# Kernel tuning notes

Hardware: AMD Instinct MI355X
Metric: run time of the kernel (lower is better)

The kernel has to match this reference:

```python
import jax, jax.numpy as jnp
import numpy as np

H = 1024      # hidden_size
NH = 16       # num_heads
HD = H // NH  # head_dim


def setup_inputs() -> dict:
    key = jax.random.key(0)
    ks = jax.random.split(key, 12)
    inp = {
        "query": jax.random.normal(ks[0], (4, 1024, H), dtype=jnp.float32),
        "key": jax.random.normal(ks[1], (4, 2048, H), dtype=jnp.float32),
        "value": jax.random.normal(ks[2], (4, 2048, H), dtype=jnp.float32),
        "key_padding_mask": jax.random.randint(ks[3], (4, 2048), 0, 2, dtype=jnp.int32),
        # learned parameters (torch Linear: y = x @ W.T + b); we store W already transposed
        "Wq": jax.random.normal(ks[4], (H, H), dtype=jnp.float32) * (1.0 / np.sqrt(H)),
        "bq": jnp.zeros((H,), dtype=jnp.float32),
        "Wk": jax.random.normal(ks[5], (H, H), dtype=jnp.float32) * (1.0 / np.sqrt(H)),
        "bk": jnp.zeros((H,), dtype=jnp.float32),
        "Wv": jax.random.normal(ks[6], (H, H), dtype=jnp.float32) * (1.0 / np.sqrt(H)),
        "bv": jnp.zeros((H,), dtype=jnp.float32),
        "Wo": jax.random.normal(ks[7], (H, H), dtype=jnp.float32) * (1.0 / np.sqrt(H)),
        "bo": jnp.zeros((H,), dtype=jnp.float32),
    }
    return inp


def reference(query, key, value, key_padding_mask, Wq, bq, Wk, bk, Wv, bv, Wo, bo):
    B, Sq, _ = query.shape
    Sk = key.shape[1]
    scaling = HD ** -0.5
    # projections -> [B, NH, S, HD]
    q = (query @ Wq + bq).reshape(B, Sq, NH, HD).transpose(0, 2, 1, 3)
    k = (key @ Wk + bk).reshape(B, Sk, NH, HD).transpose(0, 2, 1, 3)
    v = (value @ Wv + bv).reshape(B, Sk, NH, HD).transpose(0, 2, 1, 3)
    # scores [B, NH, Sq, Sk]
    scores = jnp.einsum("bhqd,bhkd->bhqk", q, k) * scaling
    # mask: positions where key_padding_mask == 0 are ignored
    scores = jnp.where((key_padding_mask == 0)[:, None, None, :], -jnp.inf, scores)
    attn = jax.nn.softmax(scores, axis=-1)
    # dropout is identity in eval mode
    out = jnp.einsum("bhqk,bhkd->bhqd", attn, v)
    out = out.transpose(0, 2, 1, 3).reshape(B, Sq, H)
    return out @ Wo + bo
```

## Files before the change

kernel.cpp:

```cpp
#include <hip/hip_runtime.h>
#include <hip/hip_fp16.h>
#include <math.h>

#define B_ 4
#define SQ 1024
#define SK 2048
#define HH 1024
#define NHEAD 16
#define HDIM 64

typedef _Float16 f16;
typedef __attribute__((ext_vector_type(8))) _Float16 f16x8;
typedef __attribute__((ext_vector_type(4))) _Float16 f16x4;
typedef __attribute__((ext_vector_type(4))) float f32x4;
typedef unsigned int u32;

#define GLOAD_LDS16(gp, lp) __builtin_amdgcn_global_load_lds( \
    (const __attribute__((address_space(1))) u32*)(gp),        \
    (__attribute__((address_space(3))) u32*)(lp), 16, 0, 0)
#define GLOAD_LDS4(gp, lp) __builtin_amdgcn_global_load_lds(  \
    (const __attribute__((address_space(1))) u32*)(gp),        \
    (__attribute__((address_space(3))) u32*)(lp), 4, 0, 0)

__global__ __launch_bounds__(256) void prep_k(
    const float* __restrict__ q, const float* __restrict__ k,
    const float* __restrict__ v,
    const float* __restrict__ W0, const float* __restrict__ W1,
    const float* __restrict__ W2, const float* __restrict__ W3,
    const int* __restrict__ mask,
    f16* __restrict__ qo, f16* __restrict__ ko, f16* __restrict__ vo,
    f16* __restrict__ WT, float* __restrict__ pbias)
{
    __shared__ f16 t[64 * 80];
    const int bid = blockIdx.x, tid = threadIdx.x;
    if (bid < 10240) {
        int i = bid * 256 + tid;
        const float* src; f16* dst; int j;
        if (i < 524288)       { src = q; dst = qo; j = i; }
        else if (i < 1572864) { src = k; dst = ko; j = i - 524288; }
        else                  { src = v; dst = vo; j = i - 1572864; }
        float4 a = ((const float4*)src)[(size_t)j * 2];
        float4 b = ((const float4*)src)[(size_t)j * 2 + 1];
        f16x8 o;
        o[0] = (f16)a.x; o[1] = (f16)a.y; o[2] = (f16)a.z; o[3] = (f16)a.w;
        o[4] = (f16)b.x; o[5] = (f16)b.y; o[6] = (f16)b.z; o[7] = (f16)b.w;
        *(f16x8*)(dst + (size_t)j * 8) = o;
    } else if (bid < 11264) {
        int id = bid - 10240;
        int z = id >> 8, idx = id & 255;
        const float* W = z == 0 ? W0 : z == 1 ? W1 : z == 2 ? W2 : W3;
        f16* out = WT + (size_t)z * HH * HH;
        const int r0 = (idx >> 4) * 64, c0 = (idx & 15) * 64;
#pragma unroll
        for (int p = 0; p < 4; p++) {
            int s = p * 256 + tid;
            int row = s >> 4, u = s & 15;
            float4 a = *(const float4*)(W + (size_t)(r0 + row) * HH + c0 + u * 4);
            f16x4 vv;
            vv[0] = (f16)a.x; vv[1] = (f16)a.y; vv[2] = (f16)a.z; vv[3] = (f16)a.w;
            *(f16x4*)(t + row * 80 + u * 4) = vv;
        }
        __syncthreads();
#pragma unroll
        for (int p = 0; p < 2; p++) {
            int s = p * 256 + tid;
            int n = s >> 3, u = s & 7;
            f16x8 vv;
#pragma unroll
            for (int j = 0; j < 8; j++) vv[j] = t[(u * 8 + j) * 80 + n];
            *(f16x8*)(out + (size_t)(c0 + n) * HH + r0 + u * 8) = vv;
        }
    } else {
        int j = (bid - 11264) * 256 + tid;
        pbias[j] = mask[j] ? 0.f : -1e30f;
    }
}

template <int TM, int OUTMODE>
__device__ __forceinline__ void gemm_body(
    const f16* __restrict__ A, const f16* __restrict__ BT,
    const float* __restrict__ bias, void* __restrict__ Cout,
    int M, int bid, int nwg, f16* sA, f16* sB)
{
    const int tid = threadIdx.x, lane = tid & 63, w = tid >> 6;
    const int swz = (bid & 7) * (nwg >> 3) + (bid >> 3);
    const int m0 = (swz >> 3) * TM;
    const int n0 = (swz & 7) * 128;
    const int wr = w >> 1, wc = w & 1;
    const int ql = lane & 15, g = lane >> 4;
    const int N = 1024, K = 1024;
    const int MF = TM / 32;
    const int ABUF = TM * 32;
    f32x4 acc[TM / 32][4] = {};

    auto stage = [&](int buf, int k0) {
#pragma unroll
        for (int p = 0; p < TM / 64; p++) {
            int s = p * 256 + tid;
            int row = s >> 2, us = ((s & 3) ^ ((row >> 1) & 3)) * 8;
            GLOAD_LDS16(A + (size_t)(m0 + row) * K + k0 + us,
                        sA + buf * ABUF + (p * 256 + w * 64) * 8);
        }
#pragma unroll
        for (int p = 0; p < 2; p++) {
            int s = p * 256 + tid;
            int row = s >> 2, us = ((s & 3) ^ ((row >> 1) & 3)) * 8;
            GLOAD_LDS16(BT + (size_t)(n0 + row) * K + k0 + us,
                        sB + buf * 4096 + (p * 256 + w * 64) * 8);
        }
    };

    stage(0, 0);
    int cur = 0;
    for (int k0 = 0; k0 < K; k0 += 32) {
        __syncthreads();
        if (k0 + 32 < K) stage(cur ^ 1, k0 + 32);
        f16x8 af[MF], bf[4];
#pragma unroll
        for (int m = 0; m < MF; m++) {
            int row = wr * (TM / 2) + m * 16 + ql;
            af[m] = *(const f16x8*)(sA + cur * ABUF + row * 32 + ((g ^ ((row >> 1) & 3)) * 8));
        }
#pragma unroll
        for (int n = 0; n < 4; n++) {
            int row = wc * 64 + n * 16 + ql;
            bf[n] = *(const f16x8*)(sB + cur * 4096 + row * 32 + ((g ^ ((row >> 1) & 3)) * 8));
        }
#pragma unroll
        for (int m = 0; m < MF; m++)
#pragma unroll
            for (int n = 0; n < 4; n++)
                acc[m][n] = __builtin_amdgcn_mfma_f32_16x16x32_f16(af[m], bf[n], acc[m][n], 0, 0, 0);
        cur ^= 1;
    }

    float bv[4];
#pragma unroll
    for (int n = 0; n < 4; n++) bv[n] = bias[n0 + wc * 64 + n * 16 + ql];
#pragma unroll
    for (int m = 0; m < MF; m++) {
        int row0 = m0 + wr * (TM / 2) + m * 16 + g * 4;
#pragma unroll
        for (int n = 0; n < 4; n++) {
            int col = n0 + wc * 64 + n * 16 + ql;
            if (OUTMODE == 2) {
                int bb = row0 >> 11, kk = row0 & 2047;
                int hh = col >> 6, dd = col & 63;
                f16x4 vv;
#pragma unroll
                for (int e = 0; e < 4; e++) vv[e] = (f16)(acc[m][n][e] + bv[n]);
                *(f16x4*)((f16*)Cout + ((size_t)(bb * NHEAD + hh) * HDIM + dd) * SK + kk) = vv;
            } else if (OUTMODE == 1) {
#pragma unroll
                for (int e = 0; e < 4; e++)
                    ((f16*)Cout)[(size_t)(row0 + e) * N + col] = (f16)(acc[m][n][e] + bv[n]);
            } else {
#pragma unroll
                for (int e = 0; e < 4; e++)
                    ((float*)Cout)[(size_t)(row0 + e) * N + col] = acc[m][n][e] + bv[n];
            }
        }
    }
}

__global__ __launch_bounds__(256) void qkv_gemm_k(
    const f16* __restrict__ qc, const f16* __restrict__ kc,
    const f16* __restrict__ vc, const f16* __restrict__ wT,
    const float* __restrict__ bq, const float* __restrict__ bk,
    const float* __restrict__ bv,
    f16* __restrict__ qp, f16* __restrict__ kp, f16* __restrict__ vt)
{
    __shared__ f16 sA[2 * 4096];
    __shared__ f16 sB[2 * 4096];
    const int bid = blockIdx.x;
    const size_t M1 = 1024 * 1024;
    if (bid < 512)
        gemm_body<64, 1>(qc, wT, bq, qp, 4096, bid, 512, sA, sB);
    else if (bid < 1024)
        gemm_body<128, 1>(kc, wT + M1, bk, kp, 8192, bid - 512, 512, sA, sB);
    else
        gemm_body<128, 2>(vc, wT + 2 * M1, bv, vt, 8192, bid - 1024, 512, sA, sB);
}

__global__ __launch_bounds__(256) void o_gemm_k(
    const f16* __restrict__ ctx, const f16* __restrict__ wT,
    const float* __restrict__ bo, float* __restrict__ out)
{
    __shared__ f16 sA[2 * 4096];
    __shared__ f16 sB[2 * 4096];
    gemm_body<64, 0>(ctx, wT, bo, out, 4096, blockIdx.x, 512, sA, sB);
}

#define SC2 0.18033688f
#define THR2 11.5f

__global__ __launch_bounds__(512, 6) void attn_mfma_k(
    const f16* __restrict__ qp,
    const f16* __restrict__ kp,
    const f16* __restrict__ vt,
    const float* __restrict__ pbias,
    f16* __restrict__ ctx)
{
    const int flat = ((int)blockIdx.x & 7) * 64 + ((int)blockIdx.x >> 3);
    const int qt = flat & 7, h = (flat >> 3) & 15, b = flat >> 7;
    const int q0 = qt * 128;
    const int tid = threadIdx.x, lane = tid & 63, w = tid >> 6;
    const int ql = lane & 15, g = lane >> 4;

    __shared__ f16 ks[2 * 4096];
    __shared__ f16 vs[2 * 4096];
    __shared__ f16 plds[8][16 * 80];
    __shared__ float sbias[2][64];

    const f16* kbase = kp + (size_t)b * SK * HH + h * HDIM;
    const f16* vbase = vt + ((size_t)(b * NHEAD + h)) * HDIM * SK;
    const float* bbase = pbias + b * SK;

    f16x8 qf[2];
    {
        const f16* qb = qp + ((size_t)(b * SQ + q0 + w * 16 + ql)) * HH + h * HDIM + g * 8;
        qf[0] = *(const f16x8*)qb;
        qf[1] = *(const f16x8*)(qb + 32);
    }

    auto stageKV = [&](int buf, int kt) {
        int r = tid >> 3, ulg = ((tid & 7) ^ (r & 7)) * 8;
        GLOAD_LDS16(kbase + (size_t)(kt + r) * HH + ulg, ks + buf * 4096 + w * 512);
        GLOAD_LDS16(vbase + (size_t)r * SK + kt + ulg,   vs + buf * 4096 + w * 512);
        if (w == 0) GLOAD_LDS4(bbase + kt + lane, &sbias[buf][0]);
    };

    f32x4 oacc[4] = {};
    float mrun = -1e30f, lrun = 0.f;

    stageKV(0, 0);
    int cur = 0;
    for (int kt = 0; kt < SK; kt += 64) {
        __syncthreads();
        if (kt + 64 < SK) stageKV(cur ^ 1, kt + 64);
        const f16* kb = ks + cur * 4096;
        const f16* vb = vs + cur * 4096;

        f32x4 sacc[4] = {};
        __builtin_amdgcn_s_setprio(1);
#pragma unroll
        for (int n = 0; n < 4; n++) {
            int key = n * 16 + ql;
#pragma unroll
            for (int df = 0; df < 2; df++) {
                int u = df * 4 + g;
                f16x8 kf = *(const f16x8*)(kb + key * 64 + ((u ^ (key & 7)) * 8));
                sacc[n] = __builtin_amdgcn_mfma_f32_16x16x32_f16(kf, qf[df], sacc[n], 0, 0, 0);
            }
        }
        __builtin_amdgcn_s_setprio(0);

        float sv[4][4];
        float mt = -1e30f;
#pragma unroll
        for (int n = 0; n < 4; n++) {
            float4 b4 = *(const float4*)&sbias[cur][n * 16 + g * 4];
            float barr[4] = {b4.x, b4.y, b4.z, b4.w};
#pragma unroll
            for (int e = 0; e < 4; e++) {
                float s = fmaf(sacc[n][e], SC2, barr[e]);
                sv[n][e] = s;
                mt = fmaxf(mt, s);
            }
        }
        mt = fmaxf(mt, __shfl_xor(mt, 16, 64));
        mt = fmaxf(mt, __shfl_xor(mt, 32, 64));

        if (__any(mt > mrun + THR2)) {
            float mnew = fmaxf(mrun, mt);
            float alpha = __builtin_amdgcn_exp2f(mrun - mnew);
            mrun = mnew;
            lrun *= alpha;
            float al[4];
#pragma unroll
            for (int e = 0; e < 4; e++) al[e] = __shfl(alpha, g * 4 + e, 64);
#pragma unroll
            for (int df = 0; df < 4; df++)
#pragma unroll
                for (int e = 0; e < 4; e++) oacc[df][e] *= al[e];
        }

        float tsum = 0.f;
#pragma unroll
        for (int n = 0; n < 4; n++) {
            float p0 = __builtin_amdgcn_exp2f(sv[n][0] - mrun);
            float p1 = __builtin_amdgcn_exp2f(sv[n][1] - mrun);
            float p2 = __builtin_amdgcn_exp2f(sv[n][2] - mrun);
            float p3 = __builtin_amdgcn_exp2f(sv[n][3] - mrun);
            tsum += (p0 + p1) + (p2 + p3);
            f16x4 pv4;
            pv4[0] = (f16)p0; pv4[1] = (f16)p1; pv4[2] = (f16)p2; pv4[3] = (f16)p3;
            *(f16x4*)(plds[w] + ql * 80 + n * 16 + g * 4) = pv4;
        }
        tsum += __shfl_xor(tsum, 16, 64);
        tsum += __shfl_xor(tsum, 32, 64);
        lrun += tsum;

        __builtin_amdgcn_s_setprio(1);
#pragma unroll
        for (int t = 0; t < 2; t++) {
            f16x8 pf = *(const f16x8*)(plds[w] + ql * 80 + t * 32 + g * 8);
#pragma unroll
            for (int df = 0; df < 4; df++) {
                int d = df * 16 + ql;
                int u = t * 4 + g;
                f16x8 vf = *(const f16x8*)(vb + d * 64 + ((u ^ (d & 7)) * 8));
                oacc[df] = __builtin_amdgcn_mfma_f32_16x16x32_f16(pf, vf, oacc[df], 0, 0, 0);
            }
        }
        __builtin_amdgcn_s_setprio(0);
        cur ^= 1;
    }

    float linv[4];
#pragma unroll
    for (int e = 0; e < 4; e++) {
        float lv = __shfl(lrun, g * 4 + e, 64);
        linv[e] = 1.f / lv;
    }
    f16* ob = ctx + ((size_t)(b * SQ + q0 + w * 16)) * HH + h * HDIM;
#pragma unroll
    for (int df = 0; df < 4; df++)
#pragma unroll
        for (int e = 0; e < 4; e++)
            ob[(size_t)(g * 4 + e) * HH + df * 16 + ql] = (f16)(oacc[df][e] * linv[e]);
}

extern "C" void kernel_launch(void* const* d_in, const int* in_sizes, int n_in,
                              void* d_out, int out_size, void* d_ws, size_t ws_size,
                              hipStream_t stream) {
    const float* query = (const float*)d_in[0];
    const float* key   = (const float*)d_in[1];
    const float* value = (const float*)d_in[2];
    const int*   mask  = (const int*)d_in[3];
    const float* Wq = (const float*)d_in[4];
    const float* bq = (const float*)d_in[5];
    const float* Wk = (const float*)d_in[6];
    const float* bk = (const float*)d_in[7];
    const float* Wv = (const float*)d_in[8];
    const float* bv = (const float*)d_in[9];
    const float* Wo = (const float*)d_in[10];
    const float* bo = (const float*)d_in[11];
    float* out = (float*)d_out;

    const size_t M1 = 1024 * 1024;
    f16* qcast = (f16*)d_ws;
    f16* kcast = qcast + 4 * M1;
    f16* vcast = kcast + 8 * M1;
    f16* wT    = vcast + 8 * M1;
    f16* qp    = wT + 4 * M1;
    f16* kp    = qp + 4 * M1;
    f16* vt    = kp + 8 * M1;
    float* pbias = (float*)(vt + 8 * M1);
    f16* ctx   = qcast;

    dim3 blk(256);

    prep_k<<<dim3(11296), blk, 0, stream>>>(query, key, value, Wq, Wk, Wv, Wo,
                                            mask, qcast, kcast, vcast, wT, pbias);

    qkv_gemm_k<<<dim3(1536), blk, 0, stream>>>(qcast, kcast, vcast, wT,
                                               bq, bk, bv, qp, kp, vt);

    attn_mfma_k<<<dim3(512), dim3(512), 0, stream>>>(qp, kp, vt, pbias, ctx);

    o_gemm_k<<<dim3(512), blk, 0, stream>>>(ctx, wT + 3 * M1, bo, out);
}
```

Before: 166.1 us.

## Unroll attention KV loop by two with static buffers, swizzle P LDS, relax occupancy

The attention loop is restructured into a lambda called twice per iteration with compile-time buffer pointers, removing the runtime cur-index arithmetic. The per-wave P staging buffer shrinks from stride 80 to 64 with an XOR swizzle, cutting LDS footprint while still avoiding bank conflicts. The launch bound's min-blocks hint drops from 6 to 4, giving the compiler more registers at the cost of possible occupancy. The GEMM body is split into stageA/stageB/compute lambdas with unroll-1 on the k loop, which is mostly a cleanup that may change scheduling.

```diff
diff --git a/kernel.cpp b/kernel.cpp
--- a/kernel.cpp
+++ b/kernel.cpp
@@ -80,7 +80,7 @@
 __device__ __forceinline__ void gemm_body(
     const f16* __restrict__ A, const f16* __restrict__ BT,
     const float* __restrict__ bias, void* __restrict__ Cout,
-    int M, int bid, int nwg, f16* sA, f16* sB)
+    int bid, int nwg, f16* sA, f16* sB)
 {
     const int tid = threadIdx.x, lane = tid & 63, w = tid >> 6;
     const int swz = (bid & 7) * (nwg >> 3) + (bid >> 3);
@@ -91,9 +91,9 @@
     const int N = 1024, K = 1024;
     const int MF = TM / 32;
     const int ABUF = TM * 32;
-    f32x4 acc[TM / 32][4] = {};
-
-    auto stage = [&](int buf, int k0) {
+    f32x4 acc[MF][4] = {};
+
+    auto stageA = [&](int buf, int k0) {
 #pragma unroll
         for (int p = 0; p < TM / 64; p++) {
             int s = p * 256 + tid;
@@ -101,6 +101,8 @@
             GLOAD_LDS16(A + (size_t)(m0 + row) * K + k0 + us,
                         sA + buf * ABUF + (p * 256 + w * 64) * 8);
         }
+    };
+    auto stageB = [&](int buf, int k0) {
 #pragma unroll
         for (int p = 0; p < 2; p++) {
             int s = p * 256 + tid;
@@ -109,28 +111,33 @@
                         sB + buf * 4096 + (p * 256 + w * 64) * 8);
         }
     };
-
-    stage(0, 0);
+    auto compute = [&](int buf) {
+        f16x8 af[MF], bf[4];
+#pragma unroll
+        for (int m = 0; m < MF; m++) {
+            int row = wr * (TM / 2) + m * 16 + ql;
+            af[m] = *(const f16x8*)(sA + buf * ABUF + row * 32 + ((g ^ ((row >> 1) & 3)) * 8));
+        }
+#pragma unroll
+        for (int n = 0; n < 4; n++) {
+            int row = wc * 64 + n * 16 + ql;
+            bf[n] = *(const f16x8*)(sB + buf * 4096 + row * 32 + ((g ^ ((row >> 1) & 3)) * 8));
+        }
+#pragma unroll
+        for (int m = 0; m < MF; m++)
+#pragma unroll
+            for (int n = 0; n < 4; n++)
+                acc[m][n] = __builtin_amdgcn_mfma_f32_16x16x32_f16(af[m], bf[n], acc[m][n], 0, 0, 0);
+    };
+
+    stageA(0, 0);
+    stageB(0, 0);
     int cur = 0;
+#pragma unroll 1
     for (int k0 = 0; k0 < K; k0 += 32) {
         __syncthreads();
-        if (k0 + 32 < K) stage(cur ^ 1, k0 + 32);
-        f16x8 af[MF], bf[4];
-#pragma unroll
-        for (int m = 0; m < MF; m++) {
-            int row = wr * (TM / 2) + m * 16 + ql;
-            af[m] = *(const f16x8*)(sA + cur * ABUF + row * 32 + ((g ^ ((row >> 1) & 3)) * 8));
-        }
-#pragma unroll
-        for (int n = 0; n < 4; n++) {
-            int row = wc * 64 + n * 16 + ql;
-            bf[n] = *(const f16x8*)(sB + cur * 4096 + row * 32 + ((g ^ ((row >> 1) & 3)) * 8));
-        }
-#pragma unroll
-        for (int m = 0; m < MF; m++)
-#pragma unroll
-            for (int n = 0; n < 4; n++)
-                acc[m][n] = __builtin_amdgcn_mfma_f32_16x16x32_f16(af[m], bf[n], acc[m][n], 0, 0, 0);
+        if (k0 + 32 < K) { stageA(cur ^ 1, k0 + 32); stageB(cur ^ 1, k0 + 32); }
+        compute(cur);
         cur ^= 1;
     }
 
@@ -175,11 +182,11 @@
     const int bid = blockIdx.x;
     const size_t M1 = 1024 * 1024;
     if (bid < 512)
-        gemm_body<64, 1>(qc, wT, bq, qp, 4096, bid, 512, sA, sB);
+        gemm_body<64, 1>(qc, wT, bq, qp, bid, 512, sA, sB);
     else if (bid < 1024)
-        gemm_body<128, 1>(kc, wT + M1, bk, kp, 8192, bid - 512, 512, sA, sB);
+        gemm_body<128, 1>(kc, wT + M1, bk, kp, bid - 512, 512, sA, sB);
     else
-        gemm_body<128, 2>(vc, wT + 2 * M1, bv, vt, 8192, bid - 1024, 512, sA, sB);
+        gemm_body<128, 2>(vc, wT + 2 * M1, bv, vt, bid - 1024, 512, sA, sB);
 }
 
 __global__ __launch_bounds__(256) void o_gemm_k(
@@ -188,13 +195,13 @@
 {
     __shared__ f16 sA[2 * 4096];
     __shared__ f16 sB[2 * 4096];
-    gemm_body<64, 0>(ctx, wT, bo, out, 4096, blockIdx.x, 512, sA, sB);
+    gemm_body<64, 0>(ctx, wT, bo, out, blockIdx.x, 512, sA, sB);
 }
 
 #define SC2 0.18033688f
 #define THR2 11.5f
 
-__global__ __launch_bounds__(512, 6) void attn_mfma_k(
+__global__ __launch_bounds__(512, 4) void attn_mfma_k(
     const f16* __restrict__ qp,
     const f16* __restrict__ kp,
     const f16* __restrict__ vt,
@@ -209,7 +216,7 @@
 
     __shared__ f16 ks[2 * 4096];
     __shared__ f16 vs[2 * 4096];
-    __shared__ f16 plds[8][16 * 80];
+    __shared__ f16 plds[8][16 * 64];
     __shared__ float sbias[2][64];
 
     const f16* kbase = kp + (size_t)b * SK * HH + h * HDIM;
@@ -232,14 +239,12 @@
 
     f32x4 oacc[4] = {};
     float mrun = -1e30f, lrun = 0.f;
-
-    stageKV(0, 0);
-    int cur = 0;
-    for (int kt = 0; kt < SK; kt += 64) {
+    f16* pw = &plds[w][0];
+
+    auto tile = [&](const f16* kb, const f16* vb, const float* sb,
+                    bool pf_en, int pbuf, int pkt) {
         __syncthreads();
-        if (kt + 64 < SK) stageKV(cur ^ 1, kt + 64);
-        const f16* kb = ks + cur * 4096;
-        const f16* vb = vs + cur * 4096;
+        if (pf_en) stageKV(pbuf, pkt);
 
         f32x4 sacc[4] = {};
         __builtin_amdgcn_s_setprio(1);
@@ -259,7 +264,7 @@
         float mt = -1e30f;
 #pragma unroll
         for (int n = 0; n < 4; n++) {
-            float4 b4 = *(const float4*)&sbias[cur][n * 16 + g * 4];
+            float4 b4 = *(const float4*)&sb[n * 16 + g * 4];
             float barr[4] = {b4.x, b4.y, b4.z, b4.w};
 #pragma unroll
             for (int e = 0; e < 4; e++) {
@@ -295,7 +300,7 @@
             tsum += (p0 + p1) + (p2 + p3);
             f16x4 pv4;
             pv4[0] = (f16)p0; pv4[1] = (f16)p1; pv4[2] = (f16)p2; pv4[3] = (f16)p3;
-            *(f16x4*)(plds[w] + ql * 80 + n * 16 + g * 4) = pv4;
+            *(f16x4*)(pw + ql * 64 + (((2 * n + (g >> 1)) ^ (ql & 7)) * 8) + (g & 1) * 4) = pv4;
         }
         tsum += __shfl_xor(tsum, 16, 64);
         tsum += __shfl_xor(tsum, 32, 64);
@@ -304,7 +309,7 @@
         __builtin_amdgcn_s_setprio(1);
 #pragma unroll
         for (int t = 0; t < 2; t++) {
-            f16x8 pf = *(const f16x8*)(plds[w] + ql * 80 + t * 32 + g * 8);
+            f16x8 pf = *(const f16x8*)(pw + ql * 64 + (((t * 4 + g) ^ (ql & 7)) * 8));
 #pragma unroll
             for (int df = 0; df < 4; df++) {
                 int d = df * 16 + ql;
@@ -314,7 +319,13 @@
             }
         }
         __builtin_amdgcn_s_setprio(0);
-        cur ^= 1;
+    };
+
+    stageKV(0, 0);
+#pragma unroll 1
+    for (int kt = 0; kt < SK; kt += 128) {
+        tile(ks, vs, sbias[0], true, 1, kt + 64);
+        tile(ks + 4096, vs + 4096, sbias[1], kt + 128 < SK, 0, kt + 128);
     }
 
     float linv[4];
```

After: 166.4 us. No clear change (+0.2%).
